# Performance work log

Measured on AMD Instinct MI355X. Metric: run time of the kernel, lower is better.

## Reference

```python
import jax, jax.numpy as jnp
import numpy as np

H = 128          # hidden size
D = 2048         # input size
B, T = 64, 256   # batch, seq_len


def _lstm_layer(x_proj, Whh, h0, c0):
    """x_proj: [B,T,4H] precomputed input projection (+ both biases).
    Returns (full hidden sequence [B,T,H], final hidden [B,H]).
    PyTorch gate order: i, f, g, o."""
    def step(carry, xt):
        h, c = carry
        g = xt + h @ Whh.T                      # [B,4H]
        i, f, gg, o = jnp.split(g, 4, axis=-1)
        i = jax.nn.sigmoid(i)
        f = jax.nn.sigmoid(f)
        gg = jnp.tanh(gg)
        o = jax.nn.sigmoid(o)
        c = f * c + i * gg
        h = o * jnp.tanh(c)
        return (h, c), h

    (hT, _), hs = jax.lax.scan(step, (h0, c0), jnp.swapaxes(x_proj, 0, 1))
    return jnp.swapaxes(hs, 0, 1), hT


def setup_inputs() -> dict:
    key = jax.random.key(0)
    ks = jax.random.split(key, 11)
    k = 1.0 / np.sqrt(H)  # torch default init bound
    u = lambda kk, shape: jax.random.uniform(kk, shape, jnp.float32, -k, k)
    return {
        "x":    jax.random.normal(ks[0], (B, T, D), jnp.float32),
        "Wih0": u(ks[1], (4 * H, D)),
        "Whh0": u(ks[2], (4 * H, H)),
        "bih0": u(ks[3], (4 * H,)),
        "bhh0": u(ks[4], (4 * H,)),
        "Wih1": u(ks[5], (4 * H, H)),
        "Whh1": u(ks[6], (4 * H, H)),
        "bih1": u(ks[7], (4 * H,)),
        "bhh1": u(ks[8], (4 * H,)),
        "Wfc":  u(ks[9], (1, H)),
        "bfc":  u(ks[10], (1,)),
    }


def reference(x, Wih0, Whh0, bih0, bhh0, Wih1, Whh1, bih1, bhh1, Wfc, bfc):
    b = x.shape[0]
    h0 = jnp.zeros((b, H), x.dtype)
    # layer 0: batch the big input GEMM across all timesteps
    xp0 = jnp.einsum('btd,gd->btg', x, Wih0) + bih0 + bhh0   # [B,T,4H]
    seq0, _ = _lstm_layer(xp0, Whh0, h0, h0)
    # layer 1 (dropout disabled in eval)
    xp1 = jnp.einsum('bth,gh->btg', seq0, Wih1) + bih1 + bhh1
    _, hT = _lstm_layer(xp1, Whh1, h0, h0)                   # h_n[-1]
    return hT @ Wfc.T + bfc                                  # [B,1]
```

## Files before the change

kernel.cpp:

```cpp
#include <hip/hip_runtime.h>
#include <math.h>

#define HH 128
#define DD 2048
#define BATCH 64
#define TT 256
#define G4 512

typedef __attribute__((ext_vector_type(8))) short bf16x8;
typedef __attribute__((ext_vector_type(4))) float f32x4;
typedef _Float16 h2 __attribute__((ext_vector_type(2)));

static __device__ __forceinline__ unsigned short f2bf_rne(float f) {
    union { float f; unsigned u; } v; v.f = f;
    unsigned r = v.u + 0x7fff + ((v.u >> 16) & 1);
    return (unsigned short)(r >> 16);
}
static __device__ __forceinline__ float bf2f(unsigned short b) {
    union { unsigned u; float f; } v; v.u = ((unsigned)b) << 16;
    return v.f;
}
static __device__ __forceinline__ float fdot2f(h2 a, h2 b, float c) {
#if __has_builtin(__builtin_amdgcn_fdot2)
    return __builtin_amdgcn_fdot2(a, b, c, false);
#else
    return fmaf((float)a[0], (float)b[0], fmaf((float)a[1], (float)b[1], c));
#endif
}
static __device__ __forceinline__ float fexp2(float x) {
#if __has_builtin(__builtin_amdgcn_exp2f)
    return __builtin_amdgcn_exp2f(x);
#else
    return exp2f(x);
#endif
}
static __device__ __forceinline__ float frcp(float x) {
#if __has_builtin(__builtin_amdgcn_rcpf)
    return __builtin_amdgcn_rcpf(x);
#else
    return 1.f / x;
#endif
}
static __device__ __forceinline__ float sigmoid_f(float x) {
    return frcp(1.f + fexp2(-1.44269504f * x));
}
static __device__ __forceinline__ float tanh_f(float x) {
    float xx = fminf(fmaxf(x, -15.f), 15.f);
    float e = fexp2(2.88539008f * xx);
    return 1.f - 2.f * frcp(e + 1.f);
}

#define PK 40

__global__ __launch_bounds__(256) void gemm_split_bf16(
    const float* __restrict__ A, const float* __restrict__ Bw,
    const float* __restrict__ b1, const float* __restrict__ b2,
    float* __restrict__ C, int M, int N, int K)
{
    __shared__ unsigned short Ah[128 * PK], Al[128 * PK];
    __shared__ unsigned short Bh[128 * PK], Bl[128 * PK];

    const int tid = threadIdx.x;
    const int l = tid & 63;
    const int w = tid >> 6;
    const int wr = w >> 1, wc = w & 1;
    const int bm = blockIdx.y, bn = blockIdx.x;

    f32x4 acc[4][4];
#pragma unroll
    for (int m = 0; m < 4; ++m)
#pragma unroll
        for (int n = 0; n < 4; ++n) acc[m][n] = f32x4{0.f, 0.f, 0.f, 0.f};

    const float* Ab = A  + (size_t)(bm * 128) * K;
    const float* Bb = Bw + (size_t)(bn * 128) * K;

    for (int k0 = 0; k0 < K; k0 += 32) {
        __syncthreads();
#pragma unroll
        for (int q = 0; q < 4; ++q) {
            int fid = tid + 256 * q;
            int r = fid >> 3;
            int kk = (fid & 7) << 2;
            float4 av = *(const float4*)(Ab + (size_t)r * K + k0 + kk);
            float4 bv = *(const float4*)(Bb + (size_t)r * K + k0 + kk);
            float a4[4] = {av.x, av.y, av.z, av.w};
            float b4[4] = {bv.x, bv.y, bv.z, bv.w};
            ushort4 ahv, alv, bhv, blv;
            unsigned short t;
            t = f2bf_rne(a4[0]); ahv.x = t; alv.x = f2bf_rne(a4[0] - bf2f(t));
            t = f2bf_rne(a4[1]); ahv.y = t; alv.y = f2bf_rne(a4[1] - bf2f(t));
            t = f2bf_rne(a4[2]); ahv.z = t; alv.z = f2bf_rne(a4[2] - bf2f(t));
            t = f2bf_rne(a4[3]); ahv.w = t; alv.w = f2bf_rne(a4[3] - bf2f(t));
            t = f2bf_rne(b4[0]); bhv.x = t; blv.x = f2bf_rne(b4[0] - bf2f(t));
            t = f2bf_rne(b4[1]); bhv.y = t; blv.y = f2bf_rne(b4[1] - bf2f(t));
            t = f2bf_rne(b4[2]); bhv.z = t; blv.z = f2bf_rne(b4[2] - bf2f(t));
            t = f2bf_rne(b4[3]); bhv.w = t; blv.w = f2bf_rne(b4[3] - bf2f(t));
            int off = r * PK + kk;
            *(ushort4*)&Ah[off] = ahv;
            *(ushort4*)&Al[off] = alv;
            *(ushort4*)&Bh[off] = bhv;
            *(ushort4*)&Bl[off] = blv;
        }
        __syncthreads();

        bf16x8 aH[4], aL[4], bH[4], bL[4];
#pragma unroll
        for (int m = 0; m < 4; ++m) {
            int row = wr * 64 + m * 16 + (l & 15);
            int off = row * PK + 8 * (l >> 4);
            aH[m] = *(const bf16x8*)&Ah[off];
            aL[m] = *(const bf16x8*)&Al[off];
        }
#pragma unroll
        for (int n = 0; n < 4; ++n) {
            int row = wc * 64 + n * 16 + (l & 15);
            int off = row * PK + 8 * (l >> 4);
            bH[n] = *(const bf16x8*)&Bh[off];
            bL[n] = *(const bf16x8*)&Bl[off];
        }
#pragma unroll
        for (int m = 0; m < 4; ++m)
#pragma unroll
            for (int n = 0; n < 4; ++n) {
                acc[m][n] = __builtin_amdgcn_mfma_f32_16x16x32_bf16(aH[m], bH[n], acc[m][n], 0, 0, 0);
                acc[m][n] = __builtin_amdgcn_mfma_f32_16x16x32_bf16(aH[m], bL[n], acc[m][n], 0, 0, 0);
                acc[m][n] = __builtin_amdgcn_mfma_f32_16x16x32_bf16(aL[m], bH[n], acc[m][n], 0, 0, 0);
            }
    }

#pragma unroll
    for (int n = 0; n < 4; ++n) {
        int cg = bn * 128 + wc * 64 + n * 16 + (l & 15);
        float bias = b1[cg] + b2[cg];
#pragma unroll
        for (int m = 0; m < 4; ++m) {
            int r0 = bm * 128 + wr * 64 + m * 16 + ((l >> 4) << 2);
            f32x4 v = acc[m][n];
#pragma unroll
            for (int i = 0; i < 4; ++i)
                C[(size_t)(r0 + i) * N + cg] = v[i] + bias;
        }
    }
}

template <bool WRITE_SEQ, bool FINAL_FC>
__global__ __launch_bounds__(128, 1) void lstm_rec_f16(
    const float* __restrict__ xp,
    const float* __restrict__ Whh,
    float* __restrict__ seq_out,
    const float* __restrict__ Wfc,
    const float* __restrict__ bfc,
    float* __restrict__ out)
{
    const int b = blockIdx.x;
    const int j = threadIdx.x;

    __shared__ alignas(16) _Float16 hbuf[2][HH];
    __shared__ float red[2];

    h2 wreg[4][64];
#pragma unroll
    for (int g = 0; g < 4; ++g) {
        const float4* wrow = (const float4*)(Whh + (size_t)(g * HH + j) * HH);
#pragma unroll
        for (int q = 0; q < 32; ++q) {
            float4 t = wrow[q];
            wreg[g][2 * q]     = h2{(_Float16)t.x, (_Float16)t.y};
            wreg[g][2 * q + 1] = h2{(_Float16)t.z, (_Float16)t.w};
        }
    }

    hbuf[0][j] = (_Float16)0.f;
    float c = 0.f, hlast = 0.f;

    const float* xb = xp + (size_t)b * TT * G4;
    float xi = xb[j], xf = xb[HH + j], xg = xb[2 * HH + j], xo = xb[3 * HH + j];
    __syncthreads();

    int cur = 0;
    for (int t = 0; t < TT; ++t) {
        const float* xn = xb + (size_t)(t + 1 < TT ? t + 1 : t) * G4;
        float ni = xn[j], nf = xn[HH + j], ng = xn[2 * HH + j], no = xn[3 * HH + j];

        float ai = xi, af = xf, ag = xg, ao = xo;
        const uint4* hp = (const uint4*)&hbuf[cur][0];
#pragma unroll
        for (int q = 0; q < 16; ++q) {
            uint4 hv = hp[q];
            union { unsigned u; h2 h; } c0, c1, c2, c3;
            c0.u = hv.x; c1.u = hv.y; c2.u = hv.z; c3.u = hv.w;
            ai = fdot2f(wreg[0][4*q+0], c0.h, ai); ai = fdot2f(wreg[0][4*q+1], c1.h, ai);
            ai = fdot2f(wreg[0][4*q+2], c2.h, ai); ai = fdot2f(wreg[0][4*q+3], c3.h, ai);
            af = fdot2f(wreg[1][4*q+0], c0.h, af); af = fdot2f(wreg[1][4*q+1], c1.h, af);
            af = fdot2f(wreg[1][4*q+2], c2.h, af); af = fdot2f(wreg[1][4*q+3], c3.h, af);
            ag = fdot2f(wreg[2][4*q+0], c0.h, ag); ag = fdot2f(wreg[2][4*q+1], c1.h, ag);
            ag = fdot2f(wreg[2][4*q+2], c2.h, ag); ag = fdot2f(wreg[2][4*q+3], c3.h, ag);
            ao = fdot2f(wreg[3][4*q+0], c0.h, ao); ao = fdot2f(wreg[3][4*q+1], c1.h, ao);
            ao = fdot2f(wreg[3][4*q+2], c2.h, ao); ao = fdot2f(wreg[3][4*q+3], c3.h, ao);
        }

        float iv = sigmoid_f(ai);
        float fv = sigmoid_f(af);
        float ov = sigmoid_f(ao);
        float gv = tanh_f(ag);
        c = fmaf(fv, c, iv * gv);
        float h = ov * tanh_f(c);

        hbuf[cur ^ 1][j] = (_Float16)h;
        if (WRITE_SEQ)
            seq_out[((size_t)b * TT + t) * HH + j] = h;
        hlast = h;
        __syncthreads();
        cur ^= 1;
        xi = ni; xf = nf; xg = ng; xo = no;
    }

    if (FINAL_FC) {
        float p = hlast * Wfc[j];
#pragma unroll
        for (int off = 32; off > 0; off >>= 1) p += __shfl_down(p, off, 64);
        if ((j & 63) == 0) red[j >> 6] = p;
        __syncthreads();
        if (j == 0) out[b] = red[0] + red[1] + bfc[0];
    }
}

extern "C" void kernel_launch(void* const* d_in, const int* in_sizes, int n_in,
                              void* d_out, int out_size, void* d_ws, size_t ws_size,
                              hipStream_t stream)
{
    const float* x    = (const float*)d_in[0];
    const float* Wih0 = (const float*)d_in[1];
    const float* Whh0 = (const float*)d_in[2];
    const float* bih0 = (const float*)d_in[3];
    const float* bhh0 = (const float*)d_in[4];
    const float* Wih1 = (const float*)d_in[5];
    const float* Whh1 = (const float*)d_in[6];
    const float* bih1 = (const float*)d_in[7];
    const float* bhh1 = (const float*)d_in[8];
    const float* Wfc  = (const float*)d_in[9];
    const float* bfc  = (const float*)d_in[10];
    float* out = (float*)d_out;

    const int M = BATCH * TT;
    float* xp  = (float*)d_ws;
    float* seq = xp + (size_t)M * G4;

    gemm_split_bf16<<<dim3(G4 / 128, M / 128), 256, 0, stream>>>(
        x, Wih0, bih0, bhh0, xp, M, G4, DD);

    lstm_rec_f16<true, false><<<BATCH, HH, 0, stream>>>(
        xp, Whh0, seq, nullptr, nullptr, nullptr);

    gemm_split_bf16<<<dim3(G4 / 128, M / 128), 256, 0, stream>>>(
        seq, Wih1, bih1, bhh1, xp, M, G4, HH);

    lstm_rec_f16<false, true><<<BATCH, HH, 0, stream>>>(
        xp, Whh1, nullptr, Wfc, bfc, out);
}
```

Measured before the change: 991.7 us.

## Batch 16 sequences per block and use MFMA for LSTM recurrence

The recurrent kernel now processes 16 batch rows per 512-thread block and computes h@Whh^T with f16 MFMA instructions instead of per-thread fdot2 loops. The GEMM output columns are permuted so that the four gates of each hidden unit are interleaved, which puts i,f,g,o for one unit into the four accumulator lanes of a single MFMA tile. This removes the serial per-thread dot products. The trade-off is fewer blocks (4 instead of 64), so fewer CUs are occupied, and a different accumulation order and precision path.

```diff
diff --git a/kernel.cpp b/kernel.cpp
--- a/kernel.cpp
+++ b/kernel.cpp
@@ -6,10 +6,12 @@
 #define BATCH 64
 #define TT 256
 #define G4 512
+#define GB 16
+#define HPAD 136
 
 typedef __attribute__((ext_vector_type(8))) short bf16x8;
 typedef __attribute__((ext_vector_type(4))) float f32x4;
-typedef _Float16 h2 __attribute__((ext_vector_type(2)));
+typedef _Float16 f16x8 __attribute__((ext_vector_type(8)));
 
 static __device__ __forceinline__ unsigned short f2bf_rne(float f) {
     union { float f; unsigned u; } v; v.f = f;
@@ -19,13 +21,6 @@
 static __device__ __forceinline__ float bf2f(unsigned short b) {
     union { unsigned u; float f; } v; v.u = ((unsigned)b) << 16;
     return v.f;
-}
-static __device__ __forceinline__ float fdot2f(h2 a, h2 b, float c) {
-#if __has_builtin(__builtin_amdgcn_fdot2)
-    return __builtin_amdgcn_fdot2(a, b, c, false);
-#else
-    return fmaf((float)a[0], (float)b[0], fmaf((float)a[1], (float)b[1], c));
-#endif
 }
 static __device__ __forceinline__ float fexp2(float x) {
 #if __has_builtin(__builtin_amdgcn_exp2f)
@@ -72,8 +67,7 @@
 #pragma unroll
         for (int n = 0; n < 4; ++n) acc[m][n] = f32x4{0.f, 0.f, 0.f, 0.f};
 
-    const float* Ab = A  + (size_t)(bm * 128) * K;
-    const float* Bb = Bw + (size_t)(bn * 128) * K;
+    const float* Ab = A + (size_t)(bm * 128) * K;
 
     for (int k0 = 0; k0 < K; k0 += 32) {
         __syncthreads();
@@ -82,8 +76,10 @@
             int fid = tid + 256 * q;
             int r = fid >> 3;
             int kk = (fid & 7) << 2;
+            int n = bn * 128 + r;
+            int orign = ((n & 3) << 7) | (n >> 2);
             float4 av = *(const float4*)(Ab + (size_t)r * K + k0 + kk);
-            float4 bv = *(const float4*)(Bb + (size_t)r * K + k0 + kk);
+            float4 bv = *(const float4*)(Bw + (size_t)orign * K + k0 + kk);
             float a4[4] = {av.x, av.y, av.z, av.w};
             float b4[4] = {bv.x, bv.y, bv.z, bv.w};
             ushort4 ahv, alv, bhv, blv;
@@ -132,7 +128,8 @@
 #pragma unroll
     for (int n = 0; n < 4; ++n) {
         int cg = bn * 128 + wc * 64 + n * 16 + (l & 15);
-        float bias = b1[cg] + b2[cg];
+        int orig = ((cg & 3) << 7) | (cg >> 2);
+        float bias = b1[orig] + b2[orig];
 #pragma unroll
         for (int m = 0; m < 4; ++m) {
             int r0 = bm * 128 + wr * 64 + m * 16 + ((l >> 4) << 2);
@@ -145,7 +142,7 @@
 }
 
 template <bool WRITE_SEQ, bool FINAL_FC>
-__global__ __launch_bounds__(128, 1) void lstm_rec_f16(
+__global__ __launch_bounds__(512) void lstm_rec_mfma(
     const float* __restrict__ xp,
     const float* __restrict__ Whh,
     float* __restrict__ seq_out,
@@ -153,76 +150,111 @@
     const float* __restrict__ bfc,
     float* __restrict__ out)
 {
-    const int b = blockIdx.x;
-    const int j = threadIdx.x;
-
-    __shared__ alignas(16) _Float16 hbuf[2][HH];
-    __shared__ float red[2];
-
-    h2 wreg[4][64];
-#pragma unroll
-    for (int g = 0; g < 4; ++g) {
-        const float4* wrow = (const float4*)(Whh + (size_t)(g * HH + j) * HH);
-#pragma unroll
-        for (int q = 0; q < 32; ++q) {
-            float4 t = wrow[q];
-            wreg[g][2 * q]     = h2{(_Float16)t.x, (_Float16)t.y};
-            wreg[g][2 * q + 1] = h2{(_Float16)t.z, (_Float16)t.w};
-        }
-    }
-
-    hbuf[0][j] = (_Float16)0.f;
-    float c = 0.f, hlast = 0.f;
-
-    const float* xb = xp + (size_t)b * TT * G4;
-    float xi = xb[j], xf = xb[HH + j], xg = xb[2 * HH + j], xo = xb[3 * HH + j];
+    const int tid = threadIdx.x;
+    const int l  = tid & 63;
+    const int w  = tid >> 6;
+    const int lb = l & 15;
+    const int lg = l >> 4;
+    const int b  = blockIdx.x * GB + lb;
+
+    __shared__ ushort hbuf[2][GB][HPAD];
+    __shared__ float red[8][GB];
+
+    for (int i = tid; i < 2 * GB * HPAD; i += 512) ((ushort*)hbuf)[i] = 0;
+
+    f16x8 wf[4][4];
+#pragma unroll
+    for (int mm = 0; mm < 4; ++mm) {
+        int rp = (w * 4 + mm) * 16 + lb;
+        int orig = ((rp & 3) << 7) | (rp >> 2);
+        const float* wr_ = Whh + (size_t)orig * HH;
+#pragma unroll
+        for (int kt = 0; kt < 4; ++kt) {
+            float4 x0 = *(const float4*)(wr_ + kt * 32 + lg * 8);
+            float4 x1 = *(const float4*)(wr_ + kt * 32 + lg * 8 + 4);
+            f16x8 f;
+            f[0] = (_Float16)x0.x; f[1] = (_Float16)x0.y;
+            f[2] = (_Float16)x0.z; f[3] = (_Float16)x0.w;
+            f[4] = (_Float16)x1.x; f[5] = (_Float16)x1.y;
+            f[6] = (_Float16)x1.z; f[7] = (_Float16)x1.w;
+            wf[mm][kt] = f;
+        }
+    }
+
+    const float* xpb = xp + (size_t)b * TT * G4;
+    float4 xq[4];
+#pragma unroll
+    for (int mm = 0; mm < 4; ++mm)
+        xq[mm] = *(const float4*)(xpb + (w * 64 + mm * 16) + lg * 4);
+
+    float c4[4] = {0.f, 0.f, 0.f, 0.f};
+    float hv[4] = {0.f, 0.f, 0.f, 0.f};
     __syncthreads();
 
     int cur = 0;
     for (int t = 0; t < TT; ++t) {
-        const float* xn = xb + (size_t)(t + 1 < TT ? t + 1 : t) * G4;
-        float ni = xn[j], nf = xn[HH + j], ng = xn[2 * HH + j], no = xn[3 * HH + j];
-
-        float ai = xi, af = xf, ag = xg, ao = xo;
-        const uint4* hp = (const uint4*)&hbuf[cur][0];
-#pragma unroll
-        for (int q = 0; q < 16; ++q) {
-            uint4 hv = hp[q];
-            union { unsigned u; h2 h; } c0, c1, c2, c3;
-            c0.u = hv.x; c1.u = hv.y; c2.u = hv.z; c3.u = hv.w;
-            ai = fdot2f(wreg[0][4*q+0], c0.h, ai); ai = fdot2f(wreg[0][4*q+1], c1.h, ai);
-            ai = fdot2f(wreg[0][4*q+2], c2.h, ai); ai = fdot2f(wreg[0][4*q+3], c3.h, ai);
-            af = fdot2f(wreg[1][4*q+0], c0.h, af); af = fdot2f(wreg[1][4*q+1], c1.h, af);
-            af = fdot2f(wreg[1][4*q+2], c2.h, af); af = fdot2f(wreg[1][4*q+3], c3.h, af);
-            ag = fdot2f(wreg[2][4*q+0], c0.h, ag); ag = fdot2f(wreg[2][4*q+1], c1.h, ag);
-            ag = fdot2f(wreg[2][4*q+2], c2.h, ag); ag = fdot2f(wreg[2][4*q+3], c3.h, ag);
-            ao = fdot2f(wreg[3][4*q+0], c0.h, ao); ao = fdot2f(wreg[3][4*q+1], c1.h, ao);
-            ao = fdot2f(wreg[3][4*q+2], c2.h, ao); ao = fdot2f(wreg[3][4*q+3], c3.h, ao);
-        }
-
-        float iv = sigmoid_f(ai);
-        float fv = sigmoid_f(af);
-        float ov = sigmoid_f(ao);
-        float gv = tanh_f(ag);
-        c = fmaf(fv, c, iv * gv);
-        float h = ov * tanh_f(c);
-
-        hbuf[cur ^ 1][j] = (_Float16)h;
-        if (WRITE_SEQ)
-            seq_out[((size_t)b * TT + t) * HH + j] = h;
-        hlast = h;
+        f16x8 bf[4];
+#pragma unroll
+        for (int kt = 0; kt < 4; ++kt) {
+            union { uint4 u; f16x8 h; } cvt;
+            cvt.u = *(const uint4*)&hbuf[cur][lb][kt * 32 + lg * 8];
+            bf[kt] = cvt.h;
+        }
+        int tn = (t + 1 < TT) ? t + 1 : t;
+        float4 xn[4];
+#pragma unroll
+        for (int mm = 0; mm < 4; ++mm)
+            xn[mm] = *(const float4*)(xpb + (size_t)tn * G4 + w * 64 + mm * 16 + lg * 4);
+
+        f32x4 acc[4];
+#pragma unroll
+        for (int mm = 0; mm < 4; ++mm)
+            acc[mm] = f32x4{xq[mm].x, xq[mm].y, xq[mm].z, xq[mm].w};
+#pragma unroll
+        for (int kt = 0; kt < 4; ++kt)
+#pragma unroll
+            for (int mm = 0; mm < 4; ++mm)
+                acc[mm] = __builtin_amdgcn_mfma_f32_16x16x32_f16(wf[mm][kt], bf[kt], acc[mm], 0, 0, 0);
+
+#pragma unroll
+        for (int mm = 0; mm < 4; ++mm) {
+            float iv = sigmoid_f(acc[mm][0]);
+            float fv = sigmoid_f(acc[mm][1]);
+            float gg = tanh_f(acc[mm][2]);
+            float ov = sigmoid_f(acc[mm][3]);
+            float c = fmaf(fv, c4[mm], iv * gg);
+            c4[mm] = c;
+            float h = ov * tanh_f(c);
+            hv[mm] = h;
+            int u = (w * 4 + mm) * 4 + lg;
+            union { _Float16 f; ushort s; } hc; hc.f = (_Float16)h;
+            hbuf[cur ^ 1][lb][u] = hc.s;
+            if (WRITE_SEQ)
+                seq_out[((size_t)b * TT + t) * HH + u] = h;
+        }
         __syncthreads();
         cur ^= 1;
-        xi = ni; xf = nf; xg = ng; xo = no;
+#pragma unroll
+        for (int mm = 0; mm < 4; ++mm) xq[mm] = xn[mm];
     }
 
     if (FINAL_FC) {
-        float p = hlast * Wfc[j];
-#pragma unroll
-        for (int off = 32; off > 0; off >>= 1) p += __shfl_down(p, off, 64);
-        if ((j & 63) == 0) red[j >> 6] = p;
-        __syncthreads();
-        if (j == 0) out[b] = red[0] + red[1] + bfc[0];
+        float p = 0.f;
+#pragma unroll
+        for (int mm = 0; mm < 4; ++mm) {
+            int u = (w * 4 + mm) * 4 + lg;
+            p = fmaf(hv[mm], Wfc[u], p);
+        }
+        p += __shfl_xor(p, 16, 64);
+        p += __shfl_xor(p, 32, 64);
+        if (l < GB) red[w][l] = p;
+        __syncthreads();
+        if (tid < GB) {
+            float s = bfc[0];
+#pragma unroll
+            for (int q = 0; q < 8; ++q) s += red[q][tid];
+            out[blockIdx.x * GB + tid] = s;
+        }
     }
 }
 
@@ -250,12 +282,12 @@
     gemm_split_bf16<<<dim3(G4 / 128, M / 128), 256, 0, stream>>>(
         x, Wih0, bih0, bhh0, xp, M, G4, DD);
 
-    lstm_rec_f16<true, false><<<BATCH, HH, 0, stream>>>(
+    lstm_rec_mfma<true, false><<<BATCH / GB, 512, 0, stream>>>(
         xp, Whh0, seq, nullptr, nullptr, nullptr);
 
     gemm_split_bf16<<<dim3(G4 / 128, M / 128), 256, 0, stream>>>(
         seq, Wih1, bih1, bhh1, xp, M, G4, HH);
 
-    lstm_rec_f16<false, true><<<BATCH, HH, 0, stream>>>(
+    lstm_rec_mfma<false, true><<<BATCH / GB, 512, 0, stream>>>(
         xp, Whh1, nullptr, Wfc, bfc, out);
 }
```

Result: slower. 1.088 ms (+9.7%).
